# Optimization experiments

Measured on AMD Instinct MI355X. Metric: run time of the kernel, lower is better.

Reference implementation:

```python
import jax, jax.numpy as jnp
import numpy as np

NB, CODES, D = 4, 1024, 64          # n_codebooks, codes_per_book, embedding_dim
B, T, H, W = 4, 8, 32, 32
COST = 0.25                          # commitment_cost


def setup_inputs() -> dict:
    key = jax.random.key(0)
    k1, k2 = jax.random.split(key)
    z = jax.random.normal(k1, (B, NB * D, T, H, W), dtype=jnp.float32)
    embeddings = jax.random.normal(k2, (NB, CODES, D), dtype=jnp.float32)
    return {"z": z, "embeddings": embeddings}


def reference(z, embeddings):
    # (B,C,T,H,W) -> (B,T,H,W,C) -> (NB, N, D) with N = B*T*H*W
    zc = jnp.moveaxis(z, 1, -1)
    flat = zc.reshape(-1, NB, D).transpose(1, 0, 2)  # (NB, N, D)
    N = flat.shape[1]

    x2 = jnp.sum(flat * flat, axis=2, keepdims=True)                 # (NB,N,1)
    e2 = jnp.sum(embeddings * embeddings, axis=2)[:, None, :]        # (NB,1,C)
    dist = x2 - 2.0 * jnp.einsum('knd,kcd->knc', flat, embeddings) + e2
    idx = jnp.argmin(dist, axis=2)                                   # (NB, N)

    # per-book embedding gather, equivalent to torch.stack([emb[i][idx[i]]], dim=-2)
    q = jax.vmap(lambda i, e: e[i])(idx, embeddings)                 # (NB, N, D)
    quantized = q.transpose(1, 0, 2).reshape(B, T, H, W, NB * D)
    quantized = jnp.moveaxis(quantized, -1, 1)                       # (B,C,T,H,W)

    encodings = jnp.moveaxis(idx.reshape(NB, B, T, H, W), 0, -1)     # (B,T,H,W,NB)

    commitment_loss = COST * jnp.mean((z - jax.lax.stop_gradient(quantized)) ** 2)
    quantized_st = z + jax.lax.stop_gradient(quantized - z)          # straight-through

    # perplexity from code usage histogram (avoids materializing one-hot)
    counts = jax.vmap(lambda i: jnp.zeros(CODES, flat.dtype).at[i].add(1.0))(idx)
    avg_probs = counts / N
    perplexity = jnp.mean(jnp.exp(-jnp.sum(avg_probs * jnp.log(avg_probs + 1e-10), axis=1)))

    return quantized_st, encodings, commitment_loss, perplexity
```

## Files before the change

### kernel.cpp

```cpp
#include <hip/hip_runtime.h>

#define NBOOKS 4
#define CODES  1024
#define DIM    64
#define NPOS   32768
#define CCH    256
#define ENC_OFF  8388608
#define LOSS_OFF 8519680
#define PERP_OFF 8519681

#define WS_E2      0
#define WS_EHI     16384
#define WS_IDX     1064960
#define WS_CNT     1589248
#define WS_PART    1605632
#define WS_FLAGCNT 1607680
#define WS_FLAGS   1607696

typedef _Float16 f16x8 __attribute__((ext_vector_type(8)));
typedef _Float16 f16x4 __attribute__((ext_vector_type(4)));
typedef float    f32x4 __attribute__((ext_vector_type(4)));

__global__ void k_eprep2(const float* __restrict__ emb, float* __restrict__ e2,
                         _Float16* __restrict__ ehi,
                         int* __restrict__ counts, int* __restrict__ flagcnt) {
    int i = blockIdx.x * 256 + threadIdx.x;
    counts[i] = 0;
    if (i < 4) flagcnt[i] = 0;
    const float4* e = (const float4*)(emb + ((size_t)i << 6));
    _Float16* hp = ehi + ((size_t)i << 6);
    float s = 0.f;
#pragma unroll
    for (int j = 0; j < 16; ++j) {
        float4 v = e[j];
        s += v.x * v.x + v.y * v.y + v.z * v.z + v.w * v.w;
        f16x4 hv;
        hv[0] = (_Float16)(-2.f * v.x);
        hv[1] = (_Float16)(-2.f * v.y);
        hv[2] = (_Float16)(-2.f * v.z);
        hv[3] = (_Float16)(-2.f * v.w);
        *(f16x4*)&hp[j * 4] = hv;
    }
    e2[i] = s;
}

__global__ void __launch_bounds__(256, 8) k_argmin_mfma(
        const float* __restrict__ z, const float* __restrict__ e2g,
        const _Float16* __restrict__ ehi,
        int* __restrict__ idxbuf, int* __restrict__ flagcnt,
        int* __restrict__ flaglist) {
    __shared__ __attribute__((aligned(16))) char sE[3][4096];

    int tid = threadIdx.x;
    int wave = tid >> 6, lane = tid & 63;
    int lrow = lane >> 4, lcol = lane & 15;
    int k = blockIdx.y;
    int posbase = blockIdx.x * 64;
    int b = posbase >> 13, s0 = posbase & 8191;
    int wb = wave * 16;

    const float* zb = z + (((size_t)(b * CCH + k * DIM)) << 13) + s0 + wb;
    f16x8 Xh[2];
#pragma unroll
    for (int kc = 0; kc < 2; ++kc) {
        f16x8 hv;
#pragma unroll
        for (int e = 0; e < 8; ++e) {
            int d = kc * 32 + lrow * 8 + e;
            hv[e] = (_Float16)zb[((size_t)d << 13) + lcol];
        }
        Xh[kc] = hv;
    }

    int r = tid >> 3;
    int q = tid & 7;
    const char* bookh = (const char*)(ehi + ((size_t)k << 16));
    const char* src0 = bookh + r * 128 + q * 16;
    int w0 = r * 128 + ((q ^ (r & 7)) << 4);

    const float* e2p = e2g + (k << 10) + lrow * 4;

    *(f16x8*)&sE[0][w0] = *(const f16x8*)(src0);
    f32x4 ce2a = *(const f32x4*)(e2p);
    f32x4 ce2b = *(const f32x4*)(e2p + 16);

    float m1f[4], m2f[4];
#pragma unroll
    for (int rr = 0; rr < 4; ++rr) { m1f[rr] = 3.4e38f; m2f[rr] = 3.4e38f; }

    int sxk = (lcol & 7);
    int o0 = ((lrow ^ sxk) << 4);
    int o1 = (((4 + lrow) ^ sxk) << 4);
    int row0 = lcol << 7;
    int row1 = (16 + lcol) << 7;

    int cur = 0, nxt = 1, fre = 2;
    for (int it = 0; it < 32; ++it) {
        __syncthreads();
        const char* sc = sE[cur];

        f16x8 eh0a = *(const f16x8*)(sc + row0 + o0);
        f16x8 eh1a = *(const f16x8*)(sc + row0 + o1);
        f16x8 eh0b = *(const f16x8*)(sc + row1 + o0);
        f16x8 eh1b = *(const f16x8*)(sc + row1 + o1);

        f16x8 nv0;
        f32x4 ne2a, ne2b;
        bool has = it < 31;
        if (has) {
            nv0 = *(const f16x8*)(src0 + (size_t)(it + 1) * 4096);
            ne2a = *(const f32x4*)(e2p + (it + 1) * 32);
            ne2b = *(const f32x4*)(e2p + (it + 1) * 32 + 16);
        }

#pragma unroll
        for (int st = 0; st < 2; ++st) {
            f16x8 eh0 = st ? eh0b : eh0a;
            f16x8 eh1 = st ? eh1b : eh1a;
            f32x4 e2v = st ? ce2b : ce2a;
            unsigned kit = (unsigned)(it * 2 + st);
            f32x4 acc = e2v;
            acc = __builtin_amdgcn_mfma_f32_16x16x32_f16(eh0, Xh[0], acc, 0, 0, 0);
            acc = __builtin_amdgcn_mfma_f32_16x16x32_f16(eh1, Xh[1], acc, 0, 0, 0);
#pragma unroll
            for (int rr = 0; rr < 4; ++rr) {
                float key = __uint_as_float(
                    (__float_as_uint(acc[rr]) & 0xFFFFFFC0u) | kit);
                m2f[rr] = __builtin_amdgcn_fmed3f(m1f[rr], m2f[rr], key);
                m1f[rr] = fminf(m1f[rr], key);
            }
        }

        if (has) {
            *(f16x8*)&sE[nxt][w0] = nv0;
            ce2a = ne2a; ce2b = ne2b;
        }
        int t = cur; cur = nxt; nxt = fre; fre = t;
    }

    float F1, F2; int I1;
    {
        float f1 = 3.4e38f, f2 = 3.4e38f; int i1 = 0;
#pragma unroll
        for (int rr = 0; rr < 4; ++rr) {
            unsigned mb = __float_as_uint(m1f[rr]);
            float f = __uint_as_float(mb & 0xFFFFFFC0u);
            int   c = (int)(mb & 63u) * 16 + lrow * 4 + rr;
            float g = __uint_as_float(__float_as_uint(m2f[rr]) & 0xFFFFFFC0u);
            bool take = (f < f1) || (f == f1 && c < i1);
            float loser = take ? f1 : f;
            f2 = fminf(fminf(f2, g), loser);
            if (take) { f1 = f; i1 = c; }
        }
        F1 = f1; F2 = f2; I1 = i1;
    }

#pragma unroll
    for (int off = 16; off < 64; off <<= 1) {
        float om1 = __shfl_xor(F1, off);
        float om2 = __shfl_xor(F2, off);
        int   oi  = __shfl_xor(I1, off);
        bool take = (om1 < F1) || (om1 == F1 && oi < I1);
        float loser = take ? F1 : om1;
        F2 = fminf(fminf(F2, om2), loser);
        if (take) { F1 = om1; I1 = oi; }
    }

    if (lane < 16) {
        int n = posbase + wb + lane;
        idxbuf[(k << 15) + n] = I1;
        float thr = fmaf(fabsf(F1), 3.2e-5f, 5.0e-2f);
        if (F2 - F1 < thr) {
            int slot = atomicAdd(&flagcnt[k], 1);
            flaglist[(k << 15) + slot] = n;
        }
    }
}

__global__ void __launch_bounds__(256) k_rescore(
        const float* __restrict__ z, const float* __restrict__ emb,
        const float* __restrict__ e2g, const int* __restrict__ flagcnt,
        const int* __restrict__ flaglist, int* __restrict__ idxbuf) {
    __shared__ __attribute__((aligned(16))) float xsh[8][64];
    __shared__ int meta[8];
    __shared__ float bm[8][256];
    __shared__ int   bx[8][256];
    int tid = threadIdx.x;
    int wave = tid >> 6, lane = tid & 63;
    int k = blockIdx.y;
    int nf = flagcnt[k];
    const f32x4* ek4 = (const f32x4*)(emb + ((size_t)k << 16));
    const float* ee  = e2g + (k << 10);

    for (int base = blockIdx.x * 8; base < nf; base += gridDim.x * 8) {
        __syncthreads();
        if (tid < 8) meta[tid] = (base + tid < nf) ? flaglist[(k << 15) + base + tid] : -1;
        __syncthreads();
        for (int j = tid; j < 512; j += 256) {
            int p = j >> 6, d = j & 63;
            int n = meta[p];
            if (n >= 0) {
                int bb = n >> 13, s = n & 8191;
                xsh[p][d] = z[(((size_t)(bb * CCH + k * DIM + d)) << 13) + s];
            }
        }
        __syncthreads();

        const f32x4* ev0 = ek4 + (size_t)(tid) * 16;
        const f32x4* ev1 = ek4 + (size_t)(256 + tid) * 16;
        const f32x4* ev2 = ek4 + (size_t)(512 + tid) * 16;
        const f32x4* ev3 = ek4 + (size_t)(768 + tid) * 16;
        float a0[8], a1[8], a2[8], a3[8];
#pragma unroll
        for (int f = 0; f < 8; ++f) { a0[f] = 0.f; a1[f] = 0.f; a2[f] = 0.f; a3[f] = 0.f; }

        f32x4 A0 = ev0[0], A1 = ev1[0], A2 = ev2[0], A3 = ev3[0];
        f32x4 B0 = ev0[1], B1 = ev1[1], B2 = ev2[1], B3 = ev3[1];
#pragma unroll 1
        for (int jj = 0; jj < 8; ++jj) {
            int j = jj * 2;
            f32x4 C0, C1, C2, C3, D0, D1, D2, D3;
            bool has = jj < 7;
            if (has) {
                C0 = ev0[j + 2]; C1 = ev1[j + 2]; C2 = ev2[j + 2]; C3 = ev3[j + 2];
                D0 = ev0[j + 3]; D1 = ev1[j + 3]; D2 = ev2[j + 3]; D3 = ev3[j + 3];
            }
#pragma unroll
            for (int f = 0; f < 8; ++f) {
                f32x4 xa = *(const f32x4*)&xsh[f][j * 4];
                f32x4 xb = *(const f32x4*)&xsh[f][j * 4 + 4];
                a0[f] = fmaf(xa[0], A0[0], a0[f]); a0[f] = fmaf(xa[1], A0[1], a0[f]);
                a0[f] = fmaf(xa[2], A0[2], a0[f]); a0[f] = fmaf(xa[3], A0[3], a0[f]);
                a1[f] = fmaf(xa[0], A1[0], a1[f]); a1[f] = fmaf(xa[1], A1[1], a1[f]);
                a1[f] = fmaf(xa[2], A1[2], a1[f]); a1[f] = fmaf(xa[3], A1[3], a1[f]);
                a2[f] = fmaf(xa[0], A2[0], a2[f]); a2[f] = fmaf(xa[1], A2[1], a2[f]);
                a2[f] = fmaf(xa[2], A2[2], a2[f]); a2[f] = fmaf(xa[3], A2[3], a2[f]);
                a3[f] = fmaf(xa[0], A3[0], a3[f]); a3[f] = fmaf(xa[1], A3[1], a3[f]);
                a3[f] = fmaf(xa[2], A3[2], a3[f]); a3[f] = fmaf(xa[3], A3[3], a3[f]);
                a0[f] = fmaf(xb[0], B0[0], a0[f]); a0[f] = fmaf(xb[1], B0[1], a0[f]);
                a0[f] = fmaf(xb[2], B0[2], a0[f]); a0[f] = fmaf(xb[3], B0[3], a0[f]);
                a1[f] = fmaf(xb[0], B1[0], a1[f]); a1[f] = fmaf(xb[1], B1[1], a1[f]);
                a1[f] = fmaf(xb[2], B1[2], a1[f]); a1[f] = fmaf(xb[3], B1[3], a1[f]);
                a2[f] = fmaf(xb[0], B2[0], a2[f]); a2[f] = fmaf(xb[1], B2[1], a2[f]);
                a2[f] = fmaf(xb[2], B2[2], a2[f]); a2[f] = fmaf(xb[3], B2[3], a2[f]);
                a3[f] = fmaf(xb[0], B3[0], a3[f]); a3[f] = fmaf(xb[1], B3[1], a3[f]);
                a3[f] = fmaf(xb[2], B3[2], a3[f]); a3[f] = fmaf(xb[3], B3[3], a3[f]);
            }
            if (has) {
                A0 = C0; A1 = C1; A2 = C2; A3 = C3;
                B0 = D0; B1 = D1; B2 = D2; B3 = D3;
            }
        }
        float e0 = ee[tid], e1 = ee[256 + tid], e2 = ee[512 + tid], e3 = ee[768 + tid];
#pragma unroll
        for (int f = 0; f < 8; ++f) {
            float best = fmaf(-2.f, a0[f], e0); int bi = tid;
            float d1 = fmaf(-2.f, a1[f], e1);
            float d2 = fmaf(-2.f, a2[f], e2);
            float d3 = fmaf(-2.f, a3[f], e3);
            if (d1 < best) { best = d1; bi = 256 + tid; }
            if (d2 < best) { best = d2; bi = 512 + tid; }
            if (d3 < best) { best = d3; bi = 768 + tid; }
            bm[f][tid] = best;
            bx[f][tid] = bi;
        }
        __syncthreads();

#pragma unroll
        for (int ff = 0; ff < 2; ++ff) {
            int f = wave + ff * 4;
            float bv = bm[f][lane]; int bi = bx[f][lane];
#pragma unroll
            for (int o = 64; o < 256; o += 64) {
                float v2 = bm[f][lane + o]; int x2 = bx[f][lane + o];
                if (v2 < bv || (v2 == bv && x2 < bi)) { bv = v2; bi = x2; }
            }
#pragma unroll
            for (int off = 1; off < 64; off <<= 1) {
                float ob = __shfl_xor(bv, off);
                int   oi = __shfl_xor(bi, off);
                if (ob < bv || (ob == bv && oi < bi)) { bv = ob; bi = oi; }
            }
            if (lane == 0 && meta[f] >= 0) idxbuf[(k << 15) + meta[f]] = bi;
        }
    }
}

__global__ void __launch_bounds__(256) k_quant(
        const float* __restrict__ z, const float* __restrict__ emb,
        const int* __restrict__ idxbuf, float* __restrict__ out,
        int* __restrict__ counts, float* __restrict__ partial) {
    int tid = threadIdx.x;
    int q = blockIdx.x * 256 + tid;
    int n0 = q * 4;
    int k = blockIdx.y;
    int b = n0 >> 13;
    int s = n0 & 8191;

    int4 bi = *(const int4*)&idxbuf[(k << 15) + n0];
    const f32x4* e0 = (const f32x4*)(emb + ((size_t)k << 16) + ((size_t)bi.x << 6));
    const f32x4* e1 = (const f32x4*)(emb + ((size_t)k << 16) + ((size_t)bi.y << 6));
    const f32x4* e2 = (const f32x4*)(emb + ((size_t)k << 16) + ((size_t)bi.z << 6));
    const f32x4* e3 = (const f32x4*)(emb + ((size_t)k << 16) + ((size_t)bi.w << 6));
    size_t base = (((size_t)(b * CCH + k * DIM)) << 13) + s;

    float sq = 0.f;
#pragma unroll
    for (int j = 0; j < 16; ++j) {
        f32x4 q0 = e0[j], q1 = e1[j], q2 = e2[j], q3 = e3[j];
#pragma unroll
        for (int i = 0; i < 4; ++i) {
            int d = j * 4 + i;
            f32x4 zv = *(const f32x4*)(z + base + ((size_t)d << 13));
            f32x4 ov = {q0[i], q1[i], q2[i], q3[i]};
            *(f32x4*)(out + base + ((size_t)d << 13)) = ov;
            f32x4 df = zv - ov;
            sq = fmaf(df[0], df[0], sq);
            sq = fmaf(df[1], df[1], sq);
            sq = fmaf(df[2], df[2], sq);
            sq = fmaf(df[3], df[3], sq);
        }
    }

    out[ENC_OFF + (size_t)(n0 + 0) * NBOOKS + k] = (float)bi.x;
    out[ENC_OFF + (size_t)(n0 + 1) * NBOOKS + k] = (float)bi.y;
    out[ENC_OFF + (size_t)(n0 + 2) * NBOOKS + k] = (float)bi.z;
    out[ENC_OFF + (size_t)(n0 + 3) * NBOOKS + k] = (float)bi.w;
    atomicAdd(&counts[(k << 10) + bi.x], 1);
    atomicAdd(&counts[(k << 10) + bi.y], 1);
    atomicAdd(&counts[(k << 10) + bi.z], 1);
    atomicAdd(&counts[(k << 10) + bi.w], 1);

    for (int off = 32; off; off >>= 1) sq += __shfl_down(sq, off, 64);
    __shared__ float red[4];
    if ((tid & 63) == 0) red[tid >> 6] = sq;
    __syncthreads();
    if (tid == 0)
        partial[blockIdx.y * gridDim.x + blockIdx.x] = (red[0] + red[1]) + (red[2] + red[3]);
}

__global__ void __launch_bounds__(256) k_fin(
        const int* __restrict__ counts, const float* __restrict__ partial,
        float* __restrict__ out) {
    __shared__ float shl[4];
    __shared__ float shp[4];
    int tid = threadIdx.x;
    int wave = tid >> 6, lane = tid & 63;

    float s = tid < 128 ? partial[tid] : 0.f;
    for (int off = 32; off; off >>= 1) s += __shfl_down(s, off, 64);
    if (lane == 0) shl[wave] = s;

    float h = 0.f;
    const int* ck = counts + (wave << 10) + lane * 16;
#pragma unroll
    for (int j = 0; j < 16; ++j) {
        float p = (float)ck[j] * (1.f / 32768.f);
        h += p * logf(p + 1e-10f);
    }
    for (int off = 32; off; off >>= 1) h += __shfl_down(h, off, 64);
    if (lane == 0) shp[wave] = expf(-h);
    __syncthreads();
    if (tid == 0) {
        out[LOSS_OFF] = 0.25f * ((shl[0] + shl[1]) + (shl[2] + shl[3])) / 8388608.f;
        out[PERP_OFF] = 0.25f * ((shp[0] + shp[1]) + (shp[2] + shp[3]));
    }
}

extern "C" void kernel_launch(void* const* d_in, const int* in_sizes, int n_in,
                              void* d_out, int out_size, void* d_ws, size_t ws_size,
                              hipStream_t stream) {
    const float* z   = (const float*)d_in[0];
    const float* emb = (const float*)d_in[1];
    float* out = (float*)d_out;
    char* ws = (char*)d_ws;

    float*    e2       = (float*)(ws + WS_E2);
    _Float16* ehi      = (_Float16*)(ws + WS_EHI);
    int*      idxbuf   = (int*)(ws + WS_IDX);
    int*      counts   = (int*)(ws + WS_CNT);
    float*    partial  = (float*)(ws + WS_PART);
    int*      flagcnt  = (int*)(ws + WS_FLAGCNT);
    int*      flaglist = (int*)(ws + WS_FLAGS);

    k_eprep2<<<16, 256, 0, stream>>>(emb, e2, ehi, counts, flagcnt);

    dim3 agrid(NPOS / 64, NBOOKS);
    k_argmin_mfma<<<agrid, 256, 0, stream>>>(z, e2, ehi, idxbuf, flagcnt, flaglist);

    dim3 rgrid(256, NBOOKS);
    k_rescore<<<rgrid, 256, 0, stream>>>(z, emb, e2, flagcnt, flaglist, idxbuf);

    dim3 qgrid(NPOS / 1024, NBOOKS);
    k_quant<<<qgrid, 256, 0, stream>>>(z, emb, idxbuf, out, counts, partial);
    k_fin<<<1, 256, 0, stream>>>(counts, partial, out);
}
```

Baseline: 107.2 us.

## Split codebook across waves, each wave scores all 64 positions from registers

```diff
diff --git a/kernel.cpp b/kernel.cpp
--- a/kernel.cpp
+++ b/kernel.cpp
@@ -44,12 +44,14 @@
     e2[i] = s;
 }
 
-__global__ void __launch_bounds__(256, 8) k_argmin_mfma(
+__global__ void __launch_bounds__(256, 5) k_argmin_mfma(
         const float* __restrict__ z, const float* __restrict__ e2g,
         const _Float16* __restrict__ ehi,
         int* __restrict__ idxbuf, int* __restrict__ flagcnt,
         int* __restrict__ flaglist) {
-    __shared__ __attribute__((aligned(16))) char sE[3][4096];
+    __shared__ float sF1[256];
+    __shared__ float sF2[256];
+    __shared__ int   sI1[256];
 
     int tid = threadIdx.x;
     int wave = tid >> 6, lane = tid & 63;
@@ -57,120 +59,117 @@
     int k = blockIdx.y;
     int posbase = blockIdx.x * 64;
     int b = posbase >> 13, s0 = posbase & 8191;
-    int wb = wave * 16;
-
-    const float* zb = z + (((size_t)(b * CCH + k * DIM)) << 13) + s0 + wb;
-    f16x8 Xh[2];
-#pragma unroll
-    for (int kc = 0; kc < 2; ++kc) {
-        f16x8 hv;
-#pragma unroll
-        for (int e = 0; e < 8; ++e) {
-            int d = kc * 32 + lrow * 8 + e;
-            hv[e] = (_Float16)zb[((size_t)d << 13) + lcol];
-        }
-        Xh[kc] = hv;
-    }
-
-    int r = tid >> 3;
-    int q = tid & 7;
-    const char* bookh = (const char*)(ehi + ((size_t)k << 16));
-    const char* src0 = bookh + r * 128 + q * 16;
-    int w0 = r * 128 + ((q ^ (r & 7)) << 4);
-
-    const float* e2p = e2g + (k << 10) + lrow * 4;
-
-    *(f16x8*)&sE[0][w0] = *(const f16x8*)(src0);
-    f32x4 ce2a = *(const f32x4*)(e2p);
-    f32x4 ce2b = *(const f32x4*)(e2p + 16);
-
-    float m1f[4], m2f[4];
-#pragma unroll
-    for (int rr = 0; rr < 4; ++rr) { m1f[rr] = 3.4e38f; m2f[rr] = 3.4e38f; }
-
-    int sxk = (lcol & 7);
-    int o0 = ((lrow ^ sxk) << 4);
-    int o1 = (((4 + lrow) ^ sxk) << 4);
-    int row0 = lcol << 7;
-    int row1 = (16 + lcol) << 7;
-
-    int cur = 0, nxt = 1, fre = 2;
-    for (int it = 0; it < 32; ++it) {
-        __syncthreads();
-        const char* sc = sE[cur];
-
-        f16x8 eh0a = *(const f16x8*)(sc + row0 + o0);
-        f16x8 eh1a = *(const f16x8*)(sc + row0 + o1);
-        f16x8 eh0b = *(const f16x8*)(sc + row1 + o0);
-        f16x8 eh1b = *(const f16x8*)(sc + row1 + o1);
-
-        f16x8 nv0;
-        f32x4 ne2a, ne2b;
-        bool has = it < 31;
+
+    const float* zb = z + (((size_t)(b * CCH + k * DIM)) << 13) + s0;
+    f16x8 Xh[4][2];
+#pragma unroll
+    for (int bt = 0; bt < 4; ++bt)
+#pragma unroll
+        for (int kc = 0; kc < 2; ++kc) {
+            f16x8 hv;
+#pragma unroll
+            for (int e = 0; e < 8; ++e) {
+                int d = kc * 32 + lrow * 8 + e;
+                hv[e] = (_Float16)zb[((size_t)d << 13) + bt * 16 + lcol];
+            }
+            Xh[bt][kc] = hv;
+        }
+
+    int slice = wave << 8;
+    const _Float16* ehp = ehi + ((size_t)k << 16)
+                        + (size_t)(slice + lcol) * 64 + lrow * 8;
+    const float*    e2p = e2g + (k << 10) + slice + lrow * 4;
+
+    f16x8 ceh0 = *(const f16x8*)(ehp);
+    f16x8 ceh1 = *(const f16x8*)(ehp + 32);
+    f32x4 ce2  = *(const f32x4*)(e2p);
+
+    float m1[4][4], m2[4];
+#pragma unroll
+    for (int bt = 0; bt < 4; ++bt) {
+        m2[bt] = 3.4e38f;
+#pragma unroll
+        for (int rr = 0; rr < 4; ++rr) m1[bt][rr] = 3.4e38f;
+    }
+
+    for (int at = 0; at < 16; ++at) {
+        f16x8 neh0, neh1;
+        f32x4 ne2;
+        bool has = at < 15;
         if (has) {
-            nv0 = *(const f16x8*)(src0 + (size_t)(it + 1) * 4096);
-            ne2a = *(const f32x4*)(e2p + (it + 1) * 32);
-            ne2b = *(const f32x4*)(e2p + (it + 1) * 32 + 16);
-        }
-
-#pragma unroll
-        for (int st = 0; st < 2; ++st) {
-            f16x8 eh0 = st ? eh0b : eh0a;
-            f16x8 eh1 = st ? eh1b : eh1a;
-            f32x4 e2v = st ? ce2b : ce2a;
-            unsigned kit = (unsigned)(it * 2 + st);
-            f32x4 acc = e2v;
-            acc = __builtin_amdgcn_mfma_f32_16x16x32_f16(eh0, Xh[0], acc, 0, 0, 0);
-            acc = __builtin_amdgcn_mfma_f32_16x16x32_f16(eh1, Xh[1], acc, 0, 0, 0);
+            const _Float16* nh = ehp + (at + 1) * 1024;
+            neh0 = *(const f16x8*)(nh);
+            neh1 = *(const f16x8*)(nh + 32);
+            ne2  = *(const f32x4*)(e2p + (at + 1) * 16);
+        }
+
+        unsigned kb = (unsigned)(at * 4);
+#pragma unroll
+        for (int bt = 0; bt < 4; ++bt) {
+            f32x4 acc = ce2;
+            acc = __builtin_amdgcn_mfma_f32_16x16x32_f16(ceh0, Xh[bt][0], acc, 0, 0, 0);
+            acc = __builtin_amdgcn_mfma_f32_16x16x32_f16(ceh1, Xh[bt][1], acc, 0, 0, 0);
 #pragma unroll
             for (int rr = 0; rr < 4; ++rr) {
                 float key = __uint_as_float(
-                    (__float_as_uint(acc[rr]) & 0xFFFFFFC0u) | kit);
-                m2f[rr] = __builtin_amdgcn_fmed3f(m1f[rr], m2f[rr], key);
-                m1f[rr] = fminf(m1f[rr], key);
-            }
-        }
-
-        if (has) {
-            *(f16x8*)&sE[nxt][w0] = nv0;
-            ce2a = ne2a; ce2b = ne2b;
-        }
-        int t = cur; cur = nxt; nxt = fre; fre = t;
-    }
-
-    float F1, F2; int I1;
-    {
-        float f1 = 3.4e38f, f2 = 3.4e38f; int i1 = 0;
-#pragma unroll
-        for (int rr = 0; rr < 4; ++rr) {
-            unsigned mb = __float_as_uint(m1f[rr]);
-            float f = __uint_as_float(mb & 0xFFFFFFC0u);
-            int   c = (int)(mb & 63u) * 16 + lrow * 4 + rr;
-            float g = __uint_as_float(__float_as_uint(m2f[rr]) & 0xFFFFFFC0u);
-            bool take = (f < f1) || (f == f1 && c < i1);
-            float loser = take ? f1 : f;
-            f2 = fminf(fminf(f2, g), loser);
-            if (take) { f1 = f; i1 = c; }
-        }
-        F1 = f1; F2 = f2; I1 = i1;
-    }
-
-#pragma unroll
-    for (int off = 16; off < 64; off <<= 1) {
-        float om1 = __shfl_xor(F1, off);
-        float om2 = __shfl_xor(F2, off);
-        int   oi  = __shfl_xor(I1, off);
-        bool take = (om1 < F1) || (om1 == F1 && oi < I1);
-        float loser = take ? F1 : om1;
-        F2 = fminf(fminf(F2, om2), loser);
-        if (take) { F1 = om1; I1 = oi; }
-    }
-
-    if (lane < 16) {
-        int n = posbase + wb + lane;
-        idxbuf[(k << 15) + n] = I1;
-        float thr = fmaf(fabsf(F1), 3.2e-5f, 5.0e-2f);
-        if (F2 - F1 < thr) {
+                    (__float_as_uint(acc[rr]) & 0xFFFFFFC0u) | (kb + (unsigned)rr));
+                m2[bt]     = __builtin_amdgcn_fmed3f(m1[bt][rr], m2[bt], key);
+                m1[bt][rr] = fminf(m1[bt][rr], key);
+            }
+        }
+        if (has) { ceh0 = neh0; ceh1 = neh1; ce2 = ne2; }
+    }
+
+#pragma unroll
+    for (int bt = 0; bt < 4; ++bt) {
+        float a = m1[bt][0], b2 = m1[bt][1], c = m1[bt][2], d = m1[bt][3];
+        float min01 = fminf(a, b2), min23 = fminf(c, d);
+        float max01 = fmaxf(a, b2), max23 = fmaxf(c, d);
+        float f1 = fminf(min01, min23);
+        float s2q = fminf(fmaxf(min01, min23), fminf(max01, max23));
+        float f2 = fminf(m2[bt], s2q);
+
+        unsigned mb = __float_as_uint(f1);
+        unsigned lm = mb & 63u;
+        int I1 = slice + (int)(lm >> 2) * 16 + lrow * 4 + (int)(lm & 3u);
+        float F1 = __uint_as_float(mb & 0xFFFFFFC0u);
+        float F2 = __uint_as_float(__float_as_uint(f2) & 0xFFFFFFC0u);
+
+#pragma unroll
+        for (int off = 16; off < 64; off <<= 1) {
+            float om1 = __shfl_xor(F1, off);
+            float om2 = __shfl_xor(F2, off);
+            int   oi  = __shfl_xor(I1, off);
+            bool take = (om1 < F1) || (om1 == F1 && oi < I1);
+            float loser = take ? F1 : om1;
+            F2 = fminf(fminf(F2, om2), loser);
+            if (take) { F1 = om1; I1 = oi; }
+        }
+        if (lane < 16) {
+            int p = bt * 16 + lane;
+            sF1[wave * 64 + p] = F1;
+            sF2[wave * 64 + p] = F2;
+            sI1[wave * 64 + p] = I1;
+        }
+    }
+    __syncthreads();
+
+    if (tid < 64) {
+        float a1 = sF1[tid], a2 = sF2[tid];
+        int   ai = sI1[tid];
+#pragma unroll
+        for (int w = 1; w < 4; ++w) {
+            float b1 = sF1[w * 64 + tid], b2 = sF2[w * 64 + tid];
+            int   bi = sI1[w * 64 + tid];
+            bool take = (b1 < a1) || (b1 == a1 && bi < ai);
+            float loser = take ? a1 : b1;
+            a2 = fminf(fminf(a2, b2), loser);
+            if (take) { a1 = b1; ai = bi; }
+        }
+        int n = posbase + tid;
+        idxbuf[(k << 15) + n] = ai;
+        float thr = fmaf(fabsf(a1), 3.2e-5f, 5.0e-2f);
+        if (a2 - a1 < thr) {
             int slot = atomicAdd(&flagcnt[k], 1);
             flaglist[(k << 15) + slot] = n;
         }
```

Result: slower. 212.5 us (+98.1%).
